# Performance work log

Measured on AMD Instinct MI355X. Metric: run time of the kernel, lower is better.

## Reference

```python
import jax, jax.numpy as jnp
import numpy as np


def setup_inputs() -> dict:
    key = jax.random.key(0)
    B, E, K = 1024, 1024, 64
    k0, k1, k2, k3, k4, k5 = jax.random.split(key, 6)
    s = 1.0 / np.sqrt(E)  # PyTorch GRU init bound
    c = jax.random.normal(k0, (B, E), dtype=jnp.float32)
    x = jax.random.normal(k1, (B, E, K), dtype=jnp.float32)
    W_ih = jax.random.uniform(k2, (3 * E, E), minval=-s, maxval=s, dtype=jnp.float32)
    W_hh = jax.random.uniform(k3, (3 * E, E), minval=-s, maxval=s, dtype=jnp.float32)
    b_ih = jax.random.uniform(k4, (3 * E,), minval=-s, maxval=s, dtype=jnp.float32)
    b_hh = jax.random.uniform(k5, (3 * E,), minval=-s, maxval=s, dtype=jnp.float32)
    return {"c": c, "x": x, "W_ih": W_ih, "W_hh": W_hh, "b_ih": b_ih, "b_hh": b_hh, "K": K}


def reference(c, x, W_ih, W_hh, b_ih, b_hh, K):
    # c: (B, E) initial hidden state; x: (B, E, T) teacher-forcing sequence.
    # Inputs actually consumed by the GRU: zeros at step 0, then x columns
    # [T-K .. T-2] at steps 1..K-1 (the torch slice at the last step is empty
    # and never used).
    B, E = c.shape
    T = x.shape[2]
    x_t = jnp.transpose(x, (2, 0, 1))  # (T, B, E)
    xs = jnp.concatenate(
        [jnp.zeros((1, B, E), dtype=x.dtype), x_t[T - K : T - 1]], axis=0
    )  # (K, B, E)

    def step(h, xk):
        gi = xk @ W_ih.T + b_ih  # (B, 3E)
        gh = h @ W_hh.T + b_hh   # (B, 3E)
        i_r, i_z, i_n = jnp.split(gi, 3, axis=-1)
        h_r, h_z, h_n = jnp.split(gh, 3, axis=-1)
        r = jax.nn.sigmoid(i_r + h_r)
        z = jax.nn.sigmoid(i_z + h_z)
        n = jnp.tanh(i_n + r * h_n)
        h_new = (1.0 - z) * n + z * h
        return h_new, h_new

    _, ys = jax.lax.scan(step, c, xs)  # ys: (K, B, E)
    y = jnp.transpose(ys, (1, 0, 2))   # (B, K, E) == torch.cat(y_out, dim=1)
    return jnp.transpose(y, (0, 2, 1))  # teacher-forcing transpose -> (B, E, K)
```

## Files before the change

### kernel.cpp

```cpp
#include <hip/hip_runtime.h>
#include <hip/hip_bf16.h>
#include <math.h>

typedef __bf16 bf16x8 __attribute__((ext_vector_type(8)));
typedef float f32x4 __attribute__((ext_vector_type(4)));
typedef unsigned short u16x8 __attribute__((ext_vector_type(8)));

#define VMW(N) asm volatile("s_waitcnt vmcnt(" #N ")" ::: "memory")
#define LGKM0  asm volatile("s_waitcnt lgkmcnt(0)" ::: "memory")
#define CFENCE asm volatile("" ::: "memory")

__device__ inline unsigned short f2b(float f) {
  union { float f; unsigned u; } v; v.f = f;
  unsigned u = v.u;
  return (unsigned short)((u + 0x7fffu + ((u >> 16) & 1u)) >> 16);
}
__device__ inline float b2f(unsigned short s) {
  union { unsigned u; float f; } v; v.u = ((unsigned)s) << 16;
  return v.f;
}
__device__ inline float sigm(float x) { return 1.f / (1.f + __expf(-x)); }
__device__ inline float tanh_f(float x) {
  float e = __expf(2.f * x);
  return 1.f - 2.f / (e + 1.f);
}
__device__ inline void gll16(const unsigned short* g, unsigned short* l) {
  __builtin_amdgcn_global_load_lds(
      (const __attribute__((address_space(1))) void*)g,
      (__attribute__((address_space(3))) void*)l, 16, 0, 0);
}
__device__ inline void gll16u(const unsigned short* g, unsigned short* l) {
  __builtin_amdgcn_global_load_lds(
      (const __attribute__((address_space(1))) void*)g,
      (__attribute__((address_space(3))) void*)l, 16, 0, 17);
}
__device__ inline void as64(unsigned short* p, unsigned long long v) {
  __hip_atomic_store((unsigned long long*)p, v, __ATOMIC_RELAXED,
                     __HIP_MEMORY_SCOPE_AGENT);
}

__global__ __launch_bounds__(256) void prep_kernel(
    const float* __restrict__ Wih, const float* __restrict__ Whh,
    const float* __restrict__ c, unsigned short* __restrict__ Wihb,
    unsigned short* __restrict__ Whhb, unsigned short* __restrict__ hbf,
    float* __restrict__ h32, long nW, long nH)
{
  long stride = (long)gridDim.x * blockDim.x;
  long t0 = (long)blockIdx.x * blockDim.x + threadIdx.x;
  for (long i = t0; i < nW; i += stride) {
    Wihb[i] = f2b(Wih[i]);
    Whhb[i] = f2b(Whh[i]);
  }
  for (long i = t0; i < nH; i += stride) {
    float v = c[i];
    h32[i] = v;
    hbf[i] = f2b(v);
  }
}

__global__ __launch_bounds__(256) void reorder_kernel(
    const unsigned short* __restrict__ Wihb, const unsigned short* __restrict__ Whhb,
    const float* __restrict__ bih, const float* __restrict__ bhh,
    unsigned short* __restrict__ Wihp, unsigned short* __restrict__ Whhp,
    float* __restrict__ bihp, float* __restrict__ bhhp, int E)
{
  int N3 = 3 * E;
  long total = (long)N3 * E;
  long stride = (long)gridDim.x * blockDim.x;
  long t0 = (long)blockIdx.x * blockDim.x + threadIdx.x;
  for (long i = t0; i < total; i += stride) {
    int rp = (int)(i / E);
    int col = (int)(i - (long)rp * E);
    int g6 = rp / 192, rem = rp - g6 * 192;
    int g = rem >> 6, elo = rem & 63;
    long src = ((long)g * E + g6 * 64 + elo) * E + col;
    Wihp[i] = Wihb[src];
    Whhp[i] = Whhb[src];
  }
  for (long i = t0; i < N3; i += stride) {
    int rp = (int)i;
    int g6 = rp / 192, rem = rp - g6 * 192;
    int g = rem >> 6, elo = rem & 63;
    bihp[i] = bih[(long)g * E + g6 * 64 + elo];
    bhhp[i] = bhh[(long)g * E + g6 * 64 + elo];
  }
}

__global__ __launch_bounds__(256) void transpose_x(
    const float* __restrict__ x, unsigned short* __restrict__ XS,
    int B, int E, int K)
{
  __shared__ float T[64][65];
  int e0 = blockIdx.x * 64;
  int b = blockIdx.y;
  int t = threadIdx.x;
  const float* xb = x + ((long)b * E + e0) * K;
#pragma unroll
  for (int i = 0; i < 4; ++i) {
    int cidx = i * 256 + t;
    int e = cidx >> 4;
    int f4 = cidx & 15;
    float4 v = *(const float4*)(xb + (long)e * K + f4 * 4);
    T[e][f4 * 4 + 0] = v.x;
    T[e][f4 * 4 + 1] = v.y;
    T[e][f4 * 4 + 2] = v.z;
    T[e][f4 * 4 + 3] = v.w;
  }
  __syncthreads();
#pragma unroll
  for (int i = 0; i < 16; ++i) {
    int cidx = i * 256 + t;
    int k = cidx >> 6;
    int e = cidx & 63;
    if (k < K - 1)
      XS[((long)(k + 1) * B + b) * E + e0 + e] = f2b(T[e][k]);
  }
}

__global__ __launch_bounds__(512, 1)
void gemm256(const unsigned short* __restrict__ A,
             const unsigned short* __restrict__ Bw,
             const float* __restrict__ bias,
             unsigned short* __restrict__ Cb,
             int M, int N, int K)
{
  __shared__ __align__(16) unsigned short sm[3 * 24576];

  int nwg = gridDim.x * gridDim.y;
  int wg = blockIdx.y * gridDim.x + blockIdx.x;
  if ((nwg & 7) == 0) { int ch = nwg >> 3; wg = (wg & 7) * ch + (wg >> 3); }
  int tx = wg % gridDim.x;
  int ty = wg / gridDim.x;

  const int tid = threadIdx.x;
  const int lane = tid & 63;
  const int wave = tid >> 6;
  const int wm = wave >> 2;
  const int wn = wave & 3;
  const int q = lane >> 4;
  const int l15 = lane & 15;

  const long a_base = (long)ty * 128 * K;
  const long b_base = (long)tx * 256 * K;

  long a_src[2]; int a_dst[2];
#pragma unroll
  for (int i = 0; i < 2; ++i) {
    int c = i * 512 + tid;
    int row = c >> 3;
    int g8 = (c & 7) ^ (row & 7);
    a_src[i] = a_base + (long)row * K + g8 * 8;
    a_dst[i] = c * 8;
  }
  long b_src[4]; int b_dst[4];
#pragma unroll
  for (int i = 0; i < 4; ++i) {
    int c = i * 512 + tid;
    int row = c >> 3;
    int g8 = (c & 7) ^ (row & 7);
    b_src[i] = b_base + (long)row * K + g8 * 8;
    b_dst[i] = c * 8;
  }

  int a_ro[4], b_ro[4];
#pragma unroll
  for (int mi = 0; mi < 4; ++mi) {
    int lr = wm * 64 + mi * 16 + l15;
    a_ro[mi] = lr * 64;
  }
#pragma unroll
  for (int ni = 0; ni < 4; ++ni) {
    int col = wn * 64 + ni * 16 + l15;
    b_ro[ni] = col * 64;
  }

  f32x4 acc[4][4] = {};

  const int NT = K >> 6;
#pragma unroll
  for (int t = 0; t < 2; ++t) {
    unsigned short* As = sm + t * 24576;
    unsigned short* Bs = As + 8192;
#pragma unroll
    for (int i = 0; i < 2; ++i) gll16(A + a_src[i] + t * 64, As + a_dst[i]);
#pragma unroll
    for (int i = 0; i < 4; ++i) gll16(Bw + b_src[i] + t * 64, Bs + b_dst[i]);
  }

  for (int kt = 0; kt < NT; ++kt) {
    if (kt >= NT - 2) VMW(0); else VMW(6);
    __builtin_amdgcn_s_barrier();
    CFENCE;
    const unsigned short* As = sm + (kt % 3) * 24576;
    const unsigned short* Bs = As + 8192;
    unsigned short* As2 = sm + ((kt + 2) % 3) * 24576;
    unsigned short* Bs2 = As2 + 8192;
    const bool st = (kt + 2 < NT);
    const int ko = (kt + 2) * 64;

    if (st) {
      gll16(A + a_src[0] + ko, As2 + a_dst[0]);
      gll16(A + a_src[1] + ko, As2 + a_dst[1]);
      gll16(Bw + b_src[0] + ko, Bs2 + b_dst[0]);
    }
    {
      const int c8 = q;
      bf16x8 af[4], bf_[4];
#pragma unroll
      for (int mi = 0; mi < 4; ++mi) {
        int lr = wm * 64 + mi * 16 + l15;
        af[mi] = *(const bf16x8*)&As[a_ro[mi] + ((c8 ^ (lr & 7)) << 3)];
      }
#pragma unroll
      for (int ni = 0; ni < 4; ++ni) {
        int col = wn * 64 + ni * 16 + l15;
        bf_[ni] = *(const bf16x8*)&Bs[b_ro[ni] + ((c8 ^ (col & 7)) << 3)];
      }
      __builtin_amdgcn_s_setprio(1);
#pragma unroll
      for (int mi = 0; mi < 4; ++mi)
#pragma unroll
        for (int ni = 0; ni < 4; ++ni)
          acc[mi][ni] = __builtin_amdgcn_mfma_f32_16x16x32_bf16(
              af[mi], bf_[ni], acc[mi][ni], 0, 0, 0);
      __builtin_amdgcn_s_setprio(0);
    }
    LGKM0;
    __builtin_amdgcn_s_barrier();
    CFENCE;
    if (st) {
      gll16(Bw + b_src[1] + ko, Bs2 + b_dst[1]);
      gll16(Bw + b_src[2] + ko, Bs2 + b_dst[2]);
      gll16(Bw + b_src[3] + ko, Bs2 + b_dst[3]);
    }
    {
      const int c8 = 4 + q;
      bf16x8 af[4], bf_[4];
#pragma unroll
      for (int mi = 0; mi < 4; ++mi) {
        int lr = wm * 64 + mi * 16 + l15;
        af[mi] = *(const bf16x8*)&As[a_ro[mi] + ((c8 ^ (lr & 7)) << 3)];
      }
#pragma unroll
      for (int ni = 0; ni < 4; ++ni) {
        int col = wn * 64 + ni * 16 + l15;
        bf_[ni] = *(const bf16x8*)&Bs[b_ro[ni] + ((c8 ^ (col & 7)) << 3)];
      }
      __builtin_amdgcn_s_setprio(1);
#pragma unroll
      for (int mi = 0; mi < 4; ++mi)
#pragma unroll
        for (int ni = 0; ni < 4; ++ni)
          acc[mi][ni] = __builtin_amdgcn_mfma_f32_16x16x32_bf16(
              af[mi], bf_[ni], acc[mi][ni], 0, 0, 0);
      __builtin_amdgcn_s_setprio(0);
    }
    LGKM0;
  }

  long crow0 = (long)ty * 128 + wm * 64;
  long ccol0 = (long)tx * 256 + wn * 64;
#pragma unroll
  for (int mi = 0; mi < 4; ++mi) {
#pragma unroll
    for (int ni = 0; ni < 4; ++ni) {
      long col = ccol0 + ni * 16 + l15;
      float bv = bias[col];
#pragma unroll
      for (int j = 0; j < 4; ++j) {
        long row = crow0 + mi * 16 + (q << 2) + j;
        Cb[row * N + col] = f2b(acc[mi][ni][j] + bv);
      }
    }
  }
}

#define BM 128
#define BN 128
#define BKS 64

template<int OUTBF>
__global__ __launch_bounds__(256)
void gemm_bt(const unsigned short* __restrict__ A,
             const unsigned short* __restrict__ Bw,
             const float* __restrict__ bias,
             float* __restrict__ Cf, unsigned short* __restrict__ Cb,
             int M, int N, int K)
{
  __shared__ __align__(16) unsigned short As[BM * BKS];
  __shared__ __align__(16) unsigned short Bs[BN * BKS];

  int nwg = gridDim.x * gridDim.y;
  int wg = blockIdx.y * gridDim.x + blockIdx.x;
  if ((nwg & 7) == 0) { int ch = nwg >> 3; wg = (wg & 7) * ch + (wg >> 3); }
  int tx = wg % gridDim.x;
  int ty = wg / gridDim.x;

  const int tid = threadIdx.x;
  const int lane = tid & 63;
  const int wave = tid >> 6;
  const int wr = wave >> 1, wc = wave & 1;

  f32x4 acc[4][4] = {};

  const long a_base = (long)ty * BM * K;
  const long b_base = (long)tx * BN * K;

  for (int kt = 0; kt < K; kt += BKS) {
    __syncthreads();
#pragma unroll
    for (int i = 0; i < 4; ++i) {
      int c = i * 256 + tid;
      int row = c >> 3, sc = c & 7;
      int gcol8 = sc ^ (row & 7);
      const unsigned short* ga = A + a_base + (long)row * K + kt + gcol8 * 8;
      const unsigned short* gb = Bw + b_base + (long)row * K + kt + gcol8 * 8;
      int cbase = (i * 256 + wave * 64) * 8;
      gll16(ga, &As[cbase]);
      gll16(gb, &Bs[cbase]);
    }
    __syncthreads();
#pragma unroll
    for (int kk = 0; kk < BKS; kk += 32) {
      int kidx = kk + ((lane >> 4) << 3);
      int c8 = kidx >> 3;
      bf16x8 af[4], bfv[4];
#pragma unroll
      for (int m = 0; m < 4; ++m) {
        int row = wr * 64 + m * 16 + (lane & 15);
        af[m] = *(const bf16x8*)&As[row * BKS + ((c8 ^ (row & 7)) << 3)];
      }
#pragma unroll
      for (int n = 0; n < 4; ++n) {
        int col = wc * 64 + n * 16 + (lane & 15);
        bfv[n] = *(const bf16x8*)&Bs[col * BKS + ((c8 ^ (col & 7)) << 3)];
      }
#pragma unroll
      for (int m = 0; m < 4; ++m)
#pragma unroll
        for (int n = 0; n < 4; ++n)
          acc[m][n] = __builtin_amdgcn_mfma_f32_16x16x32_bf16(
              af[m], bfv[n], acc[m][n], 0, 0, 0);
    }
  }

  long crow0 = (long)ty * BM + wr * 64;
  long ccol0 = (long)tx * BN + wc * 64;
#pragma unroll
  for (int m = 0; m < 4; ++m) {
#pragma unroll
    for (int n = 0; n < 4; ++n) {
      long col = ccol0 + n * 16 + (lane & 15);
      float bv = bias[col];
#pragma unroll
      for (int j = 0; j < 4; ++j) {
        long row = crow0 + m * 16 + ((lane >> 4) << 2) + j;
        float v = acc[m][n][j] + bv;
        if (OUTBF) Cb[row * N + col] = f2b(v);
        else       Cf[row * N + col] = v;
      }
    }
  }
}

__global__ __launch_bounds__(512, 1)
void gru_rec6(const unsigned short* __restrict__ GI,
              const unsigned short* __restrict__ Whp,
              const float* __restrict__ bhp,
              const unsigned short* __restrict__ h0,
              unsigned short* __restrict__ hbuf0,
              unsigned short* __restrict__ hbuf1,
              unsigned short* __restrict__ Y,
              unsigned int* __restrict__ bar,
              int B, int E, int K, int net)
{
  __shared__ __align__(16) unsigned char smem[156672];
  unsigned short* Ah  = (unsigned short*)smem;
  unsigned short* Bss = (unsigned short*)(smem + 49152);
  unsigned short* GIs = (unsigned short*)(smem + 122880);
  unsigned short* Ys  = (unsigned short*)(smem + 147456);
  float* Red = (float*)smem;

  const int N3 = 3 * E;
  const int e6 = blockIdx.x;
  const int bt = blockIdx.y;
  const int b0 = bt << 6;
  const int ec0 = e6 * 192;
  const int ecol0 = e6 << 6;
  const int rot = e6 & 15;
  const int tid = threadIdx.x;
  const int lane = tid & 63;
  const int w = tid >> 6;
  const int ew = w >> 1;
  const int kw = w & 1;
  const int q = lane >> 4;
  const int l15 = lane & 15;
  const int el = (ew << 4) + l15;
  const int c8 = (kw << 2) + q;
  const int axo = (c8 ^ (l15 & 7)) << 3;
  const int bxo = (c8 ^ (el & 7)) << 3;

  const int arow = tid >> 3;
  const int ag8 = (tid & 7) ^ (arow & 7);
  const long a_goff = (long)(b0 + arow) * E + ag8 * 8;
  const int a_dst = tid * 8;
  long b_goff[3]; int b_dst[3];
#pragma unroll
  for (int i = 0; i < 3; ++i) {
    int c = i * 512 + tid;
    int row = c >> 3;
    int g8 = (c & 7) ^ (row & 7);
    b_goff[i] = (long)(ec0 + row) * E + g8 * 8;
    b_dst[i] = c * 8;
  }
  long gi_off[3]; int gi_dst[3];
#pragma unroll
  for (int i = 0; i < 3; ++i) {
    int c = i * 512 + tid;
    int row = c / 24, cc = c - row * 24;
    gi_off[i] = (long)(b0 + row) * N3 + ec0 + cc * 8;
    gi_dst[i] = c * 8;
  }

  const float bh0 = bhp[ec0 + el];
  const float bh1 = bhp[ec0 + 64 + el];
  const float bh2 = bhp[ec0 + 128 + el];

  if (kw == 0) {
#pragma unroll
    for (int m = 0; m < 4; ++m)
#pragma unroll
      for (int j = 0; j < 4; ++j) {
        int row = m * 16 + q * 4 + j;
        Ys[row * 72 + el] = h0[(long)(b0 + row) * E + ecol0 + el];
      }
  }
  __syncthreads();

#pragma unroll
  for (int i = 0; i < 3; ++i)
    gll16(Whp + b_goff[i] + rot * 64, Bss + b_dst[i]);
#pragma unroll
  for (int i = 0; i < 3; ++i)
    gll16(Whp + b_goff[i] + ((rot + 1) & 15) * 64, Bss + 12288 + b_dst[i]);

  for (int k = 0; k < K; ++k) {
    const unsigned short* hprev = (k & 1) ? hbuf1 : hbuf0;
    unsigned short* hnext = (k & 1) ? hbuf0 : hbuf1;
    const unsigned short* GIk = GI + (long)k * B * N3;

    {
      int row = tid >> 3;
      int g8 = (tid & 7) ^ (row & 7);
      u16x8 v = *(const u16x8*)&Ys[row * 72 + g8 * 8];
      *(u16x8*)&Ah[a_dst] = v;
    }
#pragma unroll
    for (int t = 1; t < 5; ++t)
      gll16u(hprev + a_goff + ((rot + t) & 15) * 64, Ah + t * 4096 + a_dst);
#pragma unroll
    for (int i = 0; i < 3; ++i) gll16(GIk + gi_off[i], GIs + gi_dst[i]);

    f32x4 acc[4][3];
#pragma unroll
    for (int m = 0; m < 4; ++m)
#pragma unroll
      for (int g = 0; g < 3; ++g)
        acc[m][g] = (f32x4){0.f, 0.f, 0.f, 0.f};

#pragma unroll
    for (int kt = 0; kt < 16; ++kt) {
      if (kt <= 1)       VMW(10);
      else if (kt <= 11) VMW(5);
      else if (kt == 12) VMW(4);
      else if (kt == 15) VMW(0);
      else               VMW(3);
      LGKM0;
      __builtin_amdgcn_s_barrier();
      CFENCE;

      if (kt + 2 < 16) {
#pragma unroll
        for (int i = 0; i < 3; ++i)
          gll16(Whp + b_goff[i] + ((rot + kt + 2) & 15) * 64,
                Bss + ((kt + 2) % 3) * 12288 + b_dst[i]);
      }
      if (kt + 5 < 16)
        gll16u(hprev + a_goff + ((rot + kt + 5) & 15) * 64,
               Ah + ((kt + 5) % 6) * 4096 + a_dst);

      const unsigned short* Ab = Ah + (kt % 6) * 4096;
      const unsigned short* Bb = Bss + (kt % 3) * 12288;
      bf16x8 af[4], bfg[3];
#pragma unroll
      for (int m = 0; m < 4; ++m)
        af[m] = *(const bf16x8*)&Ab[(m * 16 + l15) * 64 + axo];
#pragma unroll
      for (int g = 0; g < 3; ++g)
        bfg[g] = *(const bf16x8*)&Bb[(g * 64 + el) * 64 + bxo];

      __builtin_amdgcn_s_setprio(1);
#pragma unroll
      for (int g = 0; g < 3; ++g)
#pragma unroll
        for (int m = 0; m < 4; ++m)
          acc[m][g] = __builtin_amdgcn_mfma_f32_16x16x32_bf16(
              af[m], bfg[g], acc[m][g], 0, 0, 0);
      __builtin_amdgcn_s_setprio(0);
    }

    __syncthreads();
    float* rp = &Red[((ew << 6) + lane) * 49];
    if (kw == 1) {
#pragma unroll
      for (int m = 0; m < 4; ++m)
#pragma unroll
        for (int g = 0; g < 3; ++g)
#pragma unroll
          for (int cc = 0; cc < 4; ++cc)
            rp[(m * 3 + g) * 4 + cc] = acc[m][g][cc];
    }
    __syncthreads();
    if (kw == 0) {
#pragma unroll
      for (int m = 0; m < 4; ++m) {
#pragma unroll
        for (int j = 0; j < 4; ++j) {
          int row = m * 16 + q * 4 + j;
          float ghr = acc[m][0][j] + rp[(m * 3 + 0) * 4 + j];
          float ghz = acc[m][1][j] + rp[(m * 3 + 1) * 4 + j];
          float ghn = acc[m][2][j] + rp[(m * 3 + 2) * 4 + j];
          float gr = b2f(GIs[row * 192 + el]);
          float gz = b2f(GIs[row * 192 + 64 + el]);
          float gn = b2f(GIs[row * 192 + 128 + el]);
          float hu = b2f(Ys[row * 72 + el]);
          float r = sigm(gr + ghr + bh0);
          float z = sigm(gz + ghz + bh1);
          float n = tanh_f(gn + r * (ghn + bh2));
          float hv = (1.f - z) * n + z * hu;
          Ys[row * 72 + el] = f2b(hv);
        }
      }
    }
    __syncthreads();
    {
      int row = tid >> 3, cc = tid & 7;
      u16x8 v = *(const u16x8*)&Ys[row * 72 + cc * 8];
      unsigned* pv = (unsigned*)&v;
      unsigned long long s0 = ((unsigned long long)pv[1] << 32) | pv[0];
      unsigned long long s1 = ((unsigned long long)pv[3] << 32) | pv[2];
      unsigned short* hp = hnext + (long)(b0 + row) * E + ecol0 + cc * 8;
      as64(hp, s0);
      as64(hp + 4, s1);
      *(u16x8*)(Y + ((long)k * B + b0 + row) * E + ecol0 + cc * 8) = v;
    }
    if (k + 1 < K) {
#pragma unroll
      for (int i = 0; i < 3; ++i)
        gll16(Whp + b_goff[i] + rot * 64, Bss + b_dst[i]);
#pragma unroll
      for (int i = 0; i < 3; ++i)
        gll16(Whp + b_goff[i] + ((rot + 1) & 15) * 64, Bss + 12288 + b_dst[i]);
      VMW(6);
      __builtin_amdgcn_s_barrier();
      CFENCE;
      if (tid == 0) {
        __hip_atomic_fetch_add(&bar[bt * 64], 1u, __ATOMIC_RELAXED,
                               __HIP_MEMORY_SCOPE_AGENT);
        unsigned target = (unsigned)(k + 1) * (unsigned)net;
        while (__hip_atomic_load(&bar[bt * 64], __ATOMIC_RELAXED,
                                 __HIP_MEMORY_SCOPE_AGENT) < target)
          __builtin_amdgcn_s_sleep(1);
      }
      __builtin_amdgcn_s_barrier();
      CFENCE;
    }
  }
}

template<int YMODE>
__global__ __launch_bounds__(256)
void gru_pointwise(const unsigned short* __restrict__ GIk,
                   const float* __restrict__ gh,
                   float* __restrict__ h, unsigned short* __restrict__ hbf,
                   unsigned short* __restrict__ Yb,
                   float* __restrict__ out, int k, int B, int E, int K)
{
  long i4 = ((long)blockIdx.x * blockDim.x + threadIdx.x) * 4;
  if (i4 >= (long)B * E) return;
  long b = i4 / E;
  long e = i4 - b * E;
  long g0 = b * 3 * E + e;
  ushort4 ir = *(const ushort4*)(GIk + g0);
  ushort4 iz = *(const ushort4*)(GIk + g0 + E);
  ushort4 in4 = *(const ushort4*)(GIk + g0 + 2 * E);
  float4 hr = *(const float4*)(gh + g0);
  float4 hz = *(const float4*)(gh + g0 + E);
  float4 hn = *(const float4*)(gh + g0 + 2 * E);
  float4 hv = *(const float4*)(h + i4);

  float irf[4] = { b2f(ir.x), b2f(ir.y), b2f(ir.z), b2f(ir.w) };
  float izf[4] = { b2f(iz.x), b2f(iz.y), b2f(iz.z), b2f(iz.w) };
  float inf_[4] = { b2f(in4.x), b2f(in4.y), b2f(in4.z), b2f(in4.w) };
  float hrf[4] = { hr.x, hr.y, hr.z, hr.w };
  float hzf[4] = { hz.x, hz.y, hz.z, hz.w };
  float hnf[4] = { hn.x, hn.y, hn.z, hn.w };
  float hvf[4] = { hv.x, hv.y, hv.z, hv.w };
  float hnew[4];
#pragma unroll
  for (int j = 0; j < 4; ++j) {
    float r = sigm(irf[j] + hrf[j]);
    float z = sigm(izf[j] + hzf[j]);
    float n = tanh_f(inf_[j] + r * hnf[j]);
    hnew[j] = (1.f - z) * n + z * hvf[j];
  }
  *(float4*)(h + i4) = make_float4(hnew[0], hnew[1], hnew[2], hnew[3]);
  ushort4 hb = make_ushort4(f2b(hnew[0]), f2b(hnew[1]), f2b(hnew[2]), f2b(hnew[3]));
  *(ushort4*)(hbf + i4) = hb;
  if (YMODE == 1) {
    *(ushort4*)(Yb + ((long)k * B + b) * E + e) = hb;
  } else {
    float* o = out + (b * E + e) * K + k;
    o[0] = hnew[0]; o[K] = hnew[1]; o[2 * K] = hnew[2]; o[3 * K] = hnew[3];
  }
}

__global__ __launch_bounds__(256)
void transpose_y(const unsigned short* __restrict__ Yv, float* __restrict__ out,
                 int B, int E, int K)
{
  __shared__ float T[64][65];
  int e0 = blockIdx.x * 64;
  int b = blockIdx.y;
  int t = threadIdx.x;
#pragma unroll
  for (int i = 0; i < 4; ++i) {
    int c = i * 256 + t;
    int k = c >> 4, f4 = c & 15;
    long off = ((long)k * B + b) * E + e0 + f4 * 4;
    ushort4 v = *(const ushort4*)(Yv + off);
    T[k][f4 * 4 + 0] = b2f(v.x); T[k][f4 * 4 + 1] = b2f(v.y);
    T[k][f4 * 4 + 2] = b2f(v.z); T[k][f4 * 4 + 3] = b2f(v.w);
  }
  __syncthreads();
#pragma unroll
  for (int i = 0; i < 4; ++i) {
    int c = i * 256 + t;
    int e = c >> 4, f4k = c & 15;
    float4 w;
    w.x = T[f4k * 4 + 0][e];
    w.y = T[f4k * 4 + 1][e];
    w.z = T[f4k * 4 + 2][e];
    w.w = T[f4k * 4 + 3][e];
    *(float4*)(out + ((long)b * E + e0 + e) * K + f4k * 4) = w;
  }
}

extern "C" void kernel_launch(void* const* d_in, const int* in_sizes, int n_in,
                              void* d_out, int out_size, void* d_ws, size_t ws_size,
                              hipStream_t stream)
{
  const float* c   = (const float*)d_in[0];
  const float* x   = (const float*)d_in[1];
  const float* Wih = (const float*)d_in[2];
  const float* Whh = (const float*)d_in[3];
  const float* bih = (const float*)d_in[4];
  const float* bhh = (const float*)d_in[5];
  float* out = (float*)d_out;

  long BE = in_sizes[0];
  int E = (int)(sqrtf((float)(in_sizes[2] / 3)) + 0.5f);
  int B = (int)(BE / E);
  int K = (int)(in_sizes[1] / BE);
  int N3 = 3 * E;
  long M_GI = (long)K * B;

  char* w = (char*)d_ws;
  size_t used = 0;
  auto alloc = [&](size_t bytes) -> char* {
    char* p = w + used;
    used += (bytes + 255) & ~(size_t)255;
    return p;
  };
  unsigned short* Wihb  = (unsigned short*)alloc((size_t)N3 * E * 2);
  unsigned short* Whhb  = (unsigned short*)alloc((size_t)N3 * E * 2);
  unsigned short* hb0   = (unsigned short*)alloc((size_t)B * E * 2);
  float* h32            = (float*)alloc((size_t)B * E * 4);
  float* gh             = (float*)alloc((size_t)B * N3 * 4);
  unsigned short* GIstep= (unsigned short*)alloc((size_t)B * N3 * 2);
  unsigned short* XS    = (unsigned short*)alloc((size_t)K * B * E * 2);

  size_t rem = (ws_size > used) ? ws_size - used : 0;
  size_t szW   = (((size_t)N3 * E * 2) + 255) & ~(size_t)255;
  size_t szB3  = (((size_t)N3 * 4) + 255) & ~(size_t)255;
  size_t szHb1 = (((size_t)B * E * 2) + 255) & ~(size_t)255;
  size_t szGI  = (((size_t)K * B * N3 * 2) + 255) & ~(size_t)255;
  size_t szY   = (((size_t)K * B * E * 2) + 255) & ~(size_t)255;
  int nbt = B / 64, net = E / 64;
  size_t szBar = ((size_t)nbt * 64 * 4 + 255) & ~(size_t)255;

  bool canFused = (B == 1024) && (E == 1024) &&
                  (rem >= 2 * szW + 2 * szB3 + szHb1 + szGI + szY + szBar);

  long nW = (long)N3 * E;
  prep_kernel<<<dim3(2048), dim3(256), 0, stream>>>(Wih, Whh, c, Wihb, Whhb,
                                                    hb0, h32, nW, BE);
  hipMemsetAsync(XS, 0, (size_t)B * E * 2, stream);
  transpose_x<<<dim3(E / 64, B), dim3(256), 0, stream>>>(x, XS, B, E, K);

  if (canFused) {
    unsigned short* Wihp = (unsigned short*)alloc(szW);
    unsigned short* Whhp = (unsigned short*)alloc(szW);
    float* bihp          = (float*)alloc(szB3);
    float* bhhp          = (float*)alloc(szB3);
    unsigned short* hb1  = (unsigned short*)alloc(szHb1);
    unsigned short* GI   = (unsigned short*)alloc(szGI);
    unsigned short* Yb   = (unsigned short*)alloc(szY);
    unsigned int*   bar  = (unsigned int*)alloc(szBar);

    reorder_kernel<<<dim3(2048), dim3(256), 0, stream>>>(
        Wihb, Whhb, bih, bhh, Wihp, Whhp, bihp, bhhp, E);

    gemm256<<<dim3(N3 / 256, (int)(M_GI / 128)), dim3(512), 0, stream>>>(
        XS, Wihp, bihp, GI, (int)M_GI, N3, E);
    hipMemsetAsync(bar, 0, szBar, stream);

    const unsigned short* GIc = GI;
    const unsigned short* Whhc = Whhp;
    const float* bhhc = bhhp;
    const unsigned short* h0c = hb0;
    void* args[] = { (void*)&GIc, (void*)&Whhc, (void*)&bhhc, (void*)&h0c,
                     (void*)&hb0, (void*)&hb1, (void*)&Yb,
                     (void*)&bar, (void*)&B, (void*)&E, (void*)&K, (void*)&net };
    hipError_t ce = hipLaunchCooperativeKernel(
        (const void*)gru_rec6, dim3(net, nbt), dim3(512), args, 0, stream);
    if (ce != hipSuccess) {
      (void)hipGetLastError();
      gru_rec6<<<dim3(net, nbt), dim3(512), 0, stream>>>(
          GIc, Whhc, bhhc, h0c, hb0, hb1, Yb, bar, B, E, K, net);
    }
    transpose_y<<<dim3(E / 64, B), dim3(256), 0, stream>>>(Yb, out, B, E, K);
    return;
  }

  int haveY = rem >= szY;
  unsigned short* Yb = haveY ? (unsigned short*)alloc(szY) : nullptr;
  int pgrid = (int)((BE / 4 + 255) / 256);
  for (int k = 0; k < K; ++k) {
    gemm_bt<1><<<dim3(N3 / BN, B / BM), dim3(256), 0, stream>>>(
        XS + (size_t)k * B * E, Wihb, bih, nullptr, GIstep, B, N3, E);
    gemm_bt<0><<<dim3(N3 / BN, B / BM), dim3(256), 0, stream>>>(
        hb0, Whhb, bhh, gh, nullptr, B, N3, E);
    if (haveY)
      gru_pointwise<1><<<dim3(pgrid), dim3(256), 0, stream>>>(
          GIstep, gh, h32, hb0, Yb, out, k, B, E, K);
    else
      gru_pointwise<2><<<dim3(pgrid), dim3(256), 0, stream>>>(
          GIstep, gh, h32, hb0, nullptr, out, k, B, E, K);
  }
  if (haveY)
    transpose_y<<<dim3(E / 64, B), dim3(256), 0, stream>>>(Yb, out, B, E, K);
}
```

Before: 1.502 ms.

## Replace per-step row-group barrier with per-tile readiness flags and 4-deep h ring

The recurrent GRU kernel drops the per-step counter barrier across each batch row group. Each block now waits only on the specific column tile of the previous hidden state it is about to load, polling a per-(step, row group, column block) flag. The hidden state moves from a double buffer to a 4-slot ring so that faster blocks cannot overwrite data that slower blocks still need to read. This gives finer-grained dataflow sync and overlap between blocks, at the cost of more flag polling and more flag memory. The fused path now also requires K==64.

Result: slower. 1.900 ms (+26.5%).

```diff
diff --git a/kernel.cpp b/kernel.cpp
--- a/kernel.cpp
+++ b/kernel.cpp
@@ -37,6 +37,10 @@
 __device__ inline void as64(unsigned short* p, unsigned long long v) {
   __hip_atomic_store((unsigned long long*)p, v, __ATOMIC_RELAXED,
                      __HIP_MEMORY_SCOPE_AGENT);
+}
+__device__ inline void waitflag(const unsigned int* p) {
+  while (__hip_atomic_load(p, __ATOMIC_RELAXED, __HIP_MEMORY_SCOPE_AGENT) == 0)
+    __builtin_amdgcn_s_sleep(1);
 }
 
 __global__ __launch_bounds__(256) void prep_kernel(
@@ -364,15 +368,14 @@
 }
 
 __global__ __launch_bounds__(512, 1)
-void gru_rec6(const unsigned short* __restrict__ GI,
+void gru_rec9(const unsigned short* __restrict__ GI,
               const unsigned short* __restrict__ Whp,
               const float* __restrict__ bhp,
-              const unsigned short* __restrict__ h0,
-              unsigned short* __restrict__ hbuf0,
-              unsigned short* __restrict__ hbuf1,
+              unsigned short* __restrict__ hbase,
+              long BEsz,
               unsigned short* __restrict__ Y,
-              unsigned int* __restrict__ bar,
-              int B, int E, int K, int net)
+              unsigned int* __restrict__ flag,
+              int B, int E, int K)
 {
   __shared__ __align__(16) unsigned char smem[156672];
   unsigned short* Ah  = (unsigned short*)smem;
@@ -432,7 +435,7 @@
 #pragma unroll
       for (int j = 0; j < 4; ++j) {
         int row = m * 16 + q * 4 + j;
-        Ys[row * 72 + el] = h0[(long)(b0 + row) * E + ecol0 + el];
+        Ys[row * 72 + el] = hbase[(long)(b0 + row) * E + ecol0 + el];
       }
   }
   __syncthreads();
@@ -445,9 +448,10 @@
     gll16(Whp + b_goff[i] + ((rot + 1) & 15) * 64, Bss + 12288 + b_dst[i]);
 
   for (int k = 0; k < K; ++k) {
-    const unsigned short* hprev = (k & 1) ? hbuf1 : hbuf0;
-    unsigned short* hnext = (k & 1) ? hbuf0 : hbuf1;
+    const unsigned short* hprev = hbase + (size_t)(k & 3) * BEsz;
+    unsigned short* hnext = hbase + (size_t)((k + 1) & 3) * BEsz;
     const unsigned short* GIk = GI + (long)k * B * N3;
+    const unsigned int* fstep = flag + ((long)k * 16 + bt) * 16;
 
     {
       int row = tid >> 3;
@@ -456,8 +460,11 @@
       *(u16x8*)&Ah[a_dst] = v;
     }
 #pragma unroll
-    for (int t = 1; t < 5; ++t)
-      gll16u(hprev + a_goff + ((rot + t) & 15) * 64, Ah + t * 4096 + a_dst);
+    for (int t = 1; t < 5; ++t) {
+      int c = (rot + t) & 15;
+      if (k > 0) waitflag(fstep + c);
+      gll16u(hprev + a_goff + c * 64, Ah + t * 4096 + a_dst);
+    }
 #pragma unroll
     for (int i = 0; i < 3; ++i) gll16(GIk + gi_off[i], GIs + gi_dst[i]);
 
@@ -485,9 +492,11 @@
           gll16(Whp + b_goff[i] + ((rot + kt + 2) & 15) * 64,
                 Bss + ((kt + 2) % 3) * 12288 + b_dst[i]);
       }
-      if (kt + 5 < 16)
-        gll16u(hprev + a_goff + ((rot + kt + 5) & 15) * 64,
-               Ah + ((kt + 5) % 6) * 4096 + a_dst);
+      if (kt + 5 < 16) {
+        int c = (rot + kt + 5) & 15;
+        if (k > 0) waitflag(fstep + c);
+        gll16u(hprev + a_goff + c * 64, Ah + ((kt + 5) % 6) * 4096 + a_dst);
+      }
 
       const unsigned short* Ab = Ah + (kt % 6) * 4096;
       const unsigned short* Bb = Bss + (kt % 3) * 12288;
@@ -564,16 +573,9 @@
       VMW(6);
       __builtin_amdgcn_s_barrier();
       CFENCE;
-      if (tid == 0) {
-        __hip_atomic_fetch_add(&bar[bt * 64], 1u, __ATOMIC_RELAXED,
-                               __HIP_MEMORY_SCOPE_AGENT);
-        unsigned target = (unsigned)(k + 1) * (unsigned)net;
-        while (__hip_atomic_load(&bar[bt * 64], __ATOMIC_RELAXED,
-                                 __HIP_MEMORY_SCOPE_AGENT) < target)
-          __builtin_amdgcn_s_sleep(1);
-      }
-      __builtin_amdgcn_s_barrier();
-      CFENCE;
+      if (tid == 0)
+        __hip_atomic_store(flag + ((long)(k + 1) * 16 + bt) * 16 + e6, 1u,
+                           __ATOMIC_RELAXED, __HIP_MEMORY_SCOPE_AGENT);
     }
   }
 }
@@ -682,9 +684,10 @@
     used += (bytes + 255) & ~(size_t)255;
     return p;
   };
+  size_t szHb1 = (((size_t)B * E * 2) + 255) & ~(size_t)255;
   unsigned short* Wihb  = (unsigned short*)alloc((size_t)N3 * E * 2);
   unsigned short* Whhb  = (unsigned short*)alloc((size_t)N3 * E * 2);
-  unsigned short* hb0   = (unsigned short*)alloc((size_t)B * E * 2);
+  unsigned short* hbM   = (unsigned short*)alloc(4 * szHb1);
   float* h32            = (float*)alloc((size_t)B * E * 4);
   float* gh             = (float*)alloc((size_t)B * N3 * 4);
   unsigned short* GIstep= (unsigned short*)alloc((size_t)B * N3 * 2);
@@ -693,18 +696,16 @@
   size_t rem = (ws_size > used) ? ws_size - used : 0;
   size_t szW   = (((size_t)N3 * E * 2) + 255) & ~(size_t)255;
   size_t szB3  = (((size_t)N3 * 4) + 255) & ~(size_t)255;
-  size_t szHb1 = (((size_t)B * E * 2) + 255) & ~(size_t)255;
   size_t szGI  = (((size_t)K * B * N3 * 2) + 255) & ~(size_t)255;
   size_t szY   = (((size_t)K * B * E * 2) + 255) & ~(size_t)255;
-  int nbt = B / 64, net = E / 64;
-  size_t szBar = ((size_t)nbt * 64 * 4 + 255) & ~(size_t)255;
-
-  bool canFused = (B == 1024) && (E == 1024) &&
-                  (rem >= 2 * szW + 2 * szB3 + szHb1 + szGI + szY + szBar);
+  size_t szFlag = (((size_t)(K + 1) * 16 * 16 * 4) + 255) & ~(size_t)255;
+
+  bool canFused = (B == 1024) && (E == 1024) && (K == 64) &&
+                  (rem >= 2 * szW + 2 * szB3 + szGI + szY + szFlag);
 
   long nW = (long)N3 * E;
   prep_kernel<<<dim3(2048), dim3(256), 0, stream>>>(Wih, Whh, c, Wihb, Whhb,
-                                                    hb0, h32, nW, BE);
+                                                    hbM, h32, nW, BE);
   hipMemsetAsync(XS, 0, (size_t)B * E * 2, stream);
   transpose_x<<<dim3(E / 64, B), dim3(256), 0, stream>>>(x, XS, B, E, K);
 
@@ -713,31 +714,30 @@
     unsigned short* Whhp = (unsigned short*)alloc(szW);
     float* bihp          = (float*)alloc(szB3);
     float* bhhp          = (float*)alloc(szB3);
-    unsigned short* hb1  = (unsigned short*)alloc(szHb1);
     unsigned short* GI   = (unsigned short*)alloc(szGI);
     unsigned short* Yb   = (unsigned short*)alloc(szY);
-    unsigned int*   bar  = (unsigned int*)alloc(szBar);
+    unsigned int*   flag = (unsigned int*)alloc(szFlag);
 
     reorder_kernel<<<dim3(2048), dim3(256), 0, stream>>>(
         Wihb, Whhb, bih, bhh, Wihp, Whhp, bihp, bhhp, E);
 
     gemm256<<<dim3(N3 / 256, (int)(M_GI / 128)), dim3(512), 0, stream>>>(
         XS, Wihp, bihp, GI, (int)M_GI, N3, E);
-    hipMemsetAsync(bar, 0, szBar, stream);
+    hipMemsetAsync(flag, 0, szFlag, stream);
 
     const unsigned short* GIc = GI;
     const unsigned short* Whhc = Whhp;
     const float* bhhc = bhhp;
-    const unsigned short* h0c = hb0;
-    void* args[] = { (void*)&GIc, (void*)&Whhc, (void*)&bhhc, (void*)&h0c,
-                     (void*)&hb0, (void*)&hb1, (void*)&Yb,
-                     (void*)&bar, (void*)&B, (void*)&E, (void*)&K, (void*)&net };
+    long BEsz = (long)szHb1 / 2;
+    void* args[] = { (void*)&GIc, (void*)&Whhc, (void*)&bhhc,
+                     (void*)&hbM, (void*)&BEsz, (void*)&Yb, (void*)&flag,
+                     (void*)&B, (void*)&E, (void*)&K };
     hipError_t ce = hipLaunchCooperativeKernel(
-        (const void*)gru_rec6, dim3(net, nbt), dim3(512), args, 0, stream);
+        (const void*)gru_rec9, dim3(16, 16), dim3(512), args, 0, stream);
     if (ce != hipSuccess) {
       (void)hipGetLastError();
-      gru_rec6<<<dim3(net, nbt), dim3(512), 0, stream>>>(
-          GIc, Whhc, bhhc, h0c, hb0, hb1, Yb, bar, B, E, K, net);
+      gru_rec9<<<dim3(16, 16), dim3(512), 0, stream>>>(
+          GIc, Whhc, bhhc, hbM, BEsz, Yb, flag, B, E, K);
     }
     transpose_y<<<dim3(E / 64, B), dim3(256), 0, stream>>>(Yb, out, B, E, K);
     return;
@@ -750,13 +750,13 @@
     gemm_bt<1><<<dim3(N3 / BN, B / BM), dim3(256), 0, stream>>>(
         XS + (size_t)k * B * E, Wihb, bih, nullptr, GIstep, B, N3, E);
     gemm_bt<0><<<dim3(N3 / BN, B / BM), dim3(256), 0, stream>>>(
-        hb0, Whhb, bhh, gh, nullptr, B, N3, E);
+        hbM, Whhb, bhh, gh, nullptr, B, N3, E);
     if (haveY)
       gru_pointwise<1><<<dim3(pgrid), dim3(256), 0, stream>>>(
-          GIstep, gh, h32, hb0, Yb, out, k, B, E, K);
+          GIstep, gh, h32, hbM, Yb, out, k, B, E, K);
     else
       gru_pointwise<2><<<dim3(pgrid), dim3(256), 0, stream>>>(
-          GIstep, gh, h32, hb0, nullptr, out, k, B, E, K);
+          GIstep, gh, h32, hbM, nullptr, out, k, B, E, K);
   }
   if (haveY)
     transpose_y<<<dim3(E / 64, B), dim3(256), 0, stream>>>(Yb, out, B, E, K);
```
